# Kernel optimization log

Hardware: AMD Instinct MI355X
Metric: run time of the kernel (lower is better)

## Reference

```python
import jax, jax.numpy as jnp
import numpy as np

KU, H, B, T = 512, 90, 32, 64
ALPHA = 0.5


def setup_inputs() -> dict:
    key = jax.random.key(0)
    ks = jax.random.split(key, 20)
    s = 0.1  # init scale ~ 1/sqrt(H)
    n = lambda k, shape: jax.random.normal(k, shape, jnp.float32) * s
    return {
        "questions": jax.random.randint(ks[0], (B, T), 0, KU),
        "answers": jax.random.randint(ks[1], (B, T), 0, 2 * KU),
        "response_emb": n(ks[2], (2 * KU, H)),
        "concept_emb": n(ks[3], (KU, H)),
        "nb_adj": (jax.random.uniform(ks[4], (KU, KU)) < 0.02).astype(jnp.float32),
        "succ_adj": (jax.random.uniform(ks[5], (KU, KU)) < 0.02).astype(jnp.float32),
        "Wi_self": n(ks[6], (H, 3 * H)), "Wh_self": n(ks[7], (H, 3 * H)),
        "bi_self": jnp.zeros((3 * H,), jnp.float32), "bh_self": jnp.zeros((3 * H,), jnp.float32),
        "Wi_rnn": n(ks[8], (H, 3 * H)), "Wh_rnn": n(ks[9], (H, 3 * H)),
        "bi_rnn": jnp.zeros((3 * H,), jnp.float32), "bh_rnn": jnp.zeros((3 * H,), jnp.float32),
        "W_sync": n(ks[10], (3 * H, H)), "b_sync": jnp.zeros((H,), jnp.float32),
        "W_prop": n(ks[11], (2 * H, H)), "b_prop": jnp.zeros((H,), jnp.float32),
        "W_agg": n(ks[12], (H, H)), "b_agg": jnp.zeros((H,), jnp.float32),
        "W_out": n(ks[13], (H, 1)), "b_out": jnp.zeros((1,), jnp.float32),
    }


def _gru(x, h, Wi, Wh, bi, bh):
    # standard GRU cell; works on [..., H]
    gi = x @ Wi + bi
    gh = h @ Wh + bh
    ir, iz, ig = jnp.split(gi, 3, axis=-1)
    hr, hz, hg = jnp.split(gh, 3, axis=-1)
    r = jax.nn.sigmoid(ir + hr)
    z = jax.nn.sigmoid(iz + hz)
    g = jnp.tanh(ig + r * hg)
    return (1.0 - z) * g + z * h


def reference(questions, answers, response_emb, concept_emb, nb_adj, succ_adj,
              Wi_self, Wh_self, bi_self, bh_self, Wi_rnn, Wh_rnn, bi_rnn, bh_rnn,
              W_sync, b_sync, W_prop, b_prop, W_agg, b_agg, W_out, b_out):
    batch = questions.shape[0]
    ku, hid = concept_emb.shape
    states0 = jnp.zeros((batch, ku, hid), jnp.float32)
    ce = jnp.broadcast_to(concept_emb[None], (batch, ku, hid))  # [B,K,H]
    bidx = jnp.arange(batch)

    def step(states, qa):
        q, a = qa  # [B], [B]
        self_state = states[bidx, q]                               # [B,H] gather
        next_self = _gru(response_emb[a], self_state, Wi_self, Wh_self, bi_self, bh_self)
        self_mask = jax.nn.one_hot(q, ku, dtype=states.dtype)[..., None]   # [B,K,1]
        nb_mask = nb_adj[q][..., None]                                      # [B,K,1]
        # sync: concat(states, broadcast next_self, concept embeds) -> MLP -> neighbor mask
        sync_diff = jnp.concatenate(
            [states, jnp.broadcast_to(next_self[:, None], (batch, ku, hid)), ce], axis=-1)
        sync_inf = nb_mask * jax.nn.relu(sync_diff @ W_sync + b_sync)       # [B,K,H]
        reflec = jnp.sum(sync_inf, axis=1, keepdims=True)                   # [B,1,H]
        sync_inf = sync_inf + self_mask * reflec
        # prop: (delta self state, concept emb of q) -> MLP -> successor mask
        prop_diff = jnp.concatenate([next_self - self_state, concept_emb[q]], axis=-1)  # [B,2H]
        prop_inf = jax.nn.relu(prop_diff @ W_prop + b_prop)                 # [B,H]
        prop_inf = succ_adj[q][..., None] * prop_inf[:, None]               # [B,K,H]
        inf = jax.nn.relu((ALPHA * sync_inf + (1.0 - ALPHA) * prop_inf) @ W_agg + b_agg)
        new_states = _gru(inf, states, Wi_rnn, Wh_rnn, bi_rnn, bh_rnn)      # [B,K,H]
        out = jax.nn.sigmoid(jnp.squeeze(new_states @ W_out + b_out, -1))   # [B,K]
        return new_states, out

    states, outputs = jax.lax.scan(step, states0, (questions.T, answers.T))
    return outputs, states  # outputs: [T,B,K], states: [B,K,H]
```

## Files before the change

kernel.cpp:

```cpp
#include <hip/hip_runtime.h>

#define KU 512
#define NB 32
#define NT 64
#define TIL 64
#define SLOTS 16
#define NBMAX 40

#define N_PONG   (KU * NB * 90)
#define OFF_CEB  (N_PONG)
#define OFF_GI0  (OFF_CEB + KU * 90)
#define OFF_WHTF (OFF_GI0 + 288)
#define OFF_SYF  (OFF_WHTF + 13824)
#define OFF_AGF  (OFF_SYF + 4608)
#define OFF_WIF  (OFF_AGF + 4608)

typedef short bf16x8 __attribute__((ext_vector_type(8)));
typedef float f32x4 __attribute__((ext_vector_type(4)));

__device__ __forceinline__ float sigf(float x) { return 1.0f / (1.0f + __expf(-x)); }
__device__ __forceinline__ float tanhf_(float x) {
    float e = __expf(2.0f * x);
    return 1.0f - 2.0f / (e + 1.0f);
}
__device__ __forceinline__ unsigned short f2bf(float f) {
    union { float f; unsigned u; } v; v.f = f;
    unsigned r = v.u + 0x7FFFu + ((v.u >> 16) & 1u);
    return (unsigned short)(r >> 16);
}
__device__ __forceinline__ bf16x8 cvt8(const float* p) {
    const float4 a0 = *(const float4*)p;
    const float4 a1 = *(const float4*)(p + 4);
    union { bf16x8 v; unsigned short u[8]; } fr;
    fr.u[0] = f2bf(a0.x); fr.u[1] = f2bf(a0.y); fr.u[2] = f2bf(a0.z); fr.u[3] = f2bf(a0.w);
    fr.u[4] = f2bf(a1.x); fr.u[5] = f2bf(a1.y); fr.u[6] = f2bf(a1.z); fr.u[7] = f2bf(a1.w);
    return fr.v;
}

__global__ void skt_prep(const float* __restrict__ concept_emb, const float* __restrict__ W_sync,
                         const float* __restrict__ b_sync, const float* __restrict__ Wi_rnn,
                         const float* __restrict__ Wh_rnn, const float* __restrict__ bi_rnn,
                         const float* __restrict__ b_agg, const float* __restrict__ W_agg,
                         float* __restrict__ ws) {
    const int blk = blockIdx.x, tid = threadIdx.x;
    if (blk < 128) {
        for (int rr = 0; rr < 4; ++rr) {
            const int k = blk * 4 + rr;
            if (tid < 90) {
                float acc = b_sync[tid];
                for (int kk = 0; kk < 90; ++kk)
                    acc += concept_emb[k * 90 + kk] * W_sync[(180 + kk) * 90 + tid];
                ws[OFF_CEB + k * 90 + tid] = acc;
            }
        }
    } else if (blk < 131) {
        const int g = blk - 128;
        unsigned short* p = (unsigned short*)(ws + OFF_WHTF);
        for (int idx = tid; idx < 6 * 3 * 64 * 8; idx += 256) {
            const int i = idx & 7, lane = (idx >> 3) & 63;
            const int rest = idx >> 9;
            const int kk = rest % 3, nb = rest / 3;
            const int n = nb * 16 + (lane & 15);
            const int k = kk * 32 + ((lane >> 4) << 3) + i;
            const float v = (n < 90 && k < 90) ? Wh_rnn[k * 270 + g * 90 + n] : 0.f;
            p[(size_t)g * 9216 + idx] = f2bf(v);
        }
    } else if (blk == 131) {
        for (int c = tid; c < 272; c += 256) {
            float acc = 0.f;
            if (c < 270) {
                acc = bi_rnn[c];
                for (int kk = 0; kk < 90; ++kk)
                    acc += fmaxf(b_agg[kk], 0.f) * Wi_rnn[kk * 270 + c];
            }
            ws[OFF_GI0 + c] = acc;
        }
    } else if (blk == 132) {
        unsigned short* p = (unsigned short*)(ws + OFF_SYF);
        for (int idx = tid; idx < 9216; idx += 256) {
            const int i = idx & 7, lane = (idx >> 3) & 63;
            const int rest = idx >> 9;
            const int kk = rest % 3, nt = rest / 3;
            const int n = nt * 16 + (lane & 15);
            const int k = kk * 32 + ((lane >> 4) << 3) + i;
            p[idx] = f2bf((n < 90 && k < 90) ? W_sync[k * 90 + n] : 0.f);
        }
    } else if (blk == 133) {
        unsigned short* p = (unsigned short*)(ws + OFF_AGF);
        for (int idx = tid; idx < 9216; idx += 256) {
            const int i = idx & 7, lane = (idx >> 3) & 63;
            const int rest = idx >> 9;
            const int kk = rest % 3, nt = rest / 3;
            const int n = nt * 16 + (lane & 15);
            const int k = kk * 32 + ((lane >> 4) << 3) + i;
            p[idx] = f2bf((n < 90 && k < 90) ? W_agg[k * 90 + n] : 0.f);
        }
    } else {
        unsigned short* p = (unsigned short*)(ws + OFF_WIF);
        const int i0 = (blk - 134) * 13824;
        const int i1 = (blk == 134) ? 13824 : 26112;
        for (int idx = i0 + tid; idx < i1; idx += 256) {
            const int i = idx & 7, lane = (idx >> 3) & 63;
            const int rest = idx >> 9;
            const int kk = rest % 3, nt = rest / 3;
            const int n = nt * 16 + (lane & 15);
            const int k = kk * 32 + ((lane >> 4) << 3) + i;
            p[idx] = f2bf((n < 270 && k < 90) ? Wi_rnn[k * 270 + n] : 0.f);
        }
    }
}

__global__ __launch_bounds__(512, 1) void skt_step(
    const int* __restrict__ qs, const int* __restrict__ as_,
    const float* __restrict__ response_emb, const float* __restrict__ concept_emb,
    const float* __restrict__ nb_adj, const float* __restrict__ succ_adj,
    const float* __restrict__ Wi_self, const float* __restrict__ Wh_self,
    const float* __restrict__ bi_self, const float* __restrict__ bh_self,
    const float* __restrict__ bi_rnn, const float* __restrict__ bh_rnn,
    const float* __restrict__ b_agg, const float* __restrict__ W_sync,
    const float* __restrict__ W_prop, const float* __restrict__ b_prop,
    const float* __restrict__ W_out, const float* __restrict__ b_out,
    float* __restrict__ ws, const float* __restrict__ stIn, float* __restrict__ stOut,
    float* __restrict__ out, int t) {
    __shared__ alignas(16) float hR[TIL * 100];
    __shared__ alignas(16) float hnb[NBMAX * 96];
    __shared__ alignas(16) float rfd[NBMAX * 92];
    __shared__ alignas(16) float giL[SLOTS * 273];
    __shared__ alignas(16) float actb[SLOTS * 96], infb[SLOTS * 96];
    __shared__ alignas(16) float giA[272], ghA[272];
    __shared__ alignas(16) float gi0L[273], biL[273], bhL[272];
    __shared__ alignas(16) float re[92], ssv[92], ceq[92], nsv[92], xprop[184];
    __shared__ alignas(16) float nsyL[92], pvL[92], baggL[92], woutL[92];
    __shared__ float nbw[NBMAX];
    __shared__ int nblist[NBMAX];
    __shared__ float nbvL[TIL], svL[TIL];
    __shared__ int rowslotS[TIL], listS[TIL];
    __shared__ int nactS, nnbS;

    const int tid = threadIdx.x;
    const int bb = blockIdx.x >> 3;
    const int k0 = (blockIdx.x & 7) * TIL;
    const int q = qs[bb * NT + t];
    const int a = as_[bb * NT + t];
    const bool owner = (q >= k0 && q < k0 + TIL);

    const int w8 = tid >> 6, lane = tid & 63;
    const int lr = lane & 15, lh = lane >> 4;
    const int rt = w8 & 3, cg = w8 >> 2;

    const unsigned short* whtF = (const unsigned short*)(ws + OFF_WHTF);
    const unsigned short* syF = (const unsigned short*)(ws + OFF_SYF);
    const unsigned short* agF = (const unsigned short*)(ws + OFF_AGF);
    const unsigned short* wiF = (const unsigned short*)(ws + OFF_WIF);

    if (tid < 384) {
        for (int idx = tid; idx < TIL * 50; idx += 384) {
            const int row = idx / 50, c2 = idx - row * 50;
            float2 v = make_float2(0.f, 0.f);
            if (c2 < 45)
                v = ((const float2*)(stIn + ((size_t)(bb * KU + k0 + row)) * 90))[c2];
            *(float2*)&hR[row * 100 + 2 * c2] = v;
        }
    } else if (tid < 448) {
        const int l = tid - 384;
        const int kg = k0 + l;
        const float nv = nb_adj[(size_t)q * KU + kg];
        const float sv = succ_adj[(size_t)q * KU + kg];
        nbvL[l] = nv; svL[l] = sv;
        const bool act = (nv != 0.f) || (sv != 0.f) || (kg == q);
        const unsigned long long mb = __ballot(act);
        const int rank = (int)__popcll(mb & ((1ull << l) - 1ull));
        rowslotS[l] = act ? rank : -1;
        if (act) listS[rank] = l;
        if (l == 0) nactS = (int)__popcll(mb);
    } else {
        const int l = tid - 448;
        int base = 0;
        for (int ch = 0; ch < 8; ++ch) {
            const int kp = ch * 64 + l;
            const float nv = nb_adj[(size_t)q * KU + kp];
            const unsigned long long mb = __ballot(nv != 0.f);
            const int idx = base + (int)__popcll(mb & ((1ull << l) - 1ull));
            if (nv != 0.f && idx < NBMAX) { nblist[idx] = kp; nbw[idx] = nv; }
            base += (int)__popcll(mb);
        }
        if (l == 0) nnbS = (base < NBMAX) ? base : NBMAX;
    }
    for (int j = tid; j < 270; j += 512) {
        if (j < 90) re[j] = response_emb[(size_t)a * 90 + j];
        else if (j < 180) ssv[j - 90] = stIn[((size_t)(bb * KU + q)) * 90 + (j - 90)];
        else ceq[j - 180] = concept_emb[(size_t)q * 90 + (j - 180)];
    }
    for (int c = tid; c < 273; c += 512) {
        gi0L[c] = (c < 272) ? ws[OFF_GI0 + c] : 0.f;
        biL[c] = (c < 270) ? bi_rnn[c] : 0.f;
        if (c < 272) bhL[c] = (c < 270) ? bh_rnn[c] : 0.f;
    }
    for (int m = tid; m < 92; m += 512) {
        baggL[m] = (m < 90) ? b_agg[m] : 0.f;
        woutL[m] = (m < 90) ? W_out[m] : 0.f;
    }
    for (int i = tid; i < SLOTS * 12; i += 512) {
        const int half = i >= SLOTS * 6;
        const int j = half ? i - SLOTS * 6 : i;
        const int slot = j / 6, c = 90 + (j - (j / 6) * 6);
        (half ? infb : actb)[slot * 96 + c] = 0.f;
    }
    __syncthreads();

    if (tid < 270) {
        const int half = tid / 135;
        const int c2 = tid - half * 135;
        const float* W = half ? Wh_self : Wi_self;
        const float* xv = half ? ssv : re;
        const float* bv = half ? bh_self : bi_self;
        float a0 = bv[2 * c2], a1 = bv[2 * c2 + 1];
#pragma unroll 15
        for (int k = 0; k < 90; ++k) {
            const float2 w = *(const float2*)&W[k * 270 + 2 * c2];
            const float x = xv[k];
            a0 += x * w.x; a1 += x * w.y;
        }
        float* dst = half ? ghA : giA;
        dst[2 * c2] = a0; dst[2 * c2 + 1] = a1;
    } else if (owner) {
        const int nnb = nnbS;
        for (int i = tid - 270; i < nnb * 48; i += 242) {
            const int j = i / 48, c2 = i - j * 48;
            float2 v = make_float2(0.f, 0.f);
            if (c2 < 45)
                v = ((const float2*)(stIn + ((size_t)(bb * KU + nblist[j])) * 90))[c2];
            *(float2*)&hnb[j * 96 + 2 * c2] = v;
        }
    }
    f32x4 acc[3][3];
#pragma unroll
    for (int g = 0; g < 3; ++g)
#pragma unroll
        for (int ct = 0; ct < 3; ++ct) acc[g][ct] = f32x4{0.f, 0.f, 0.f, 0.f};
    {
        bf16x8 afr[3];
        const float* ar = &hR[(rt * 16 + lr) * 100];
#pragma unroll
        for (int kk = 0; kk < 3; ++kk) afr[kk] = cvt8(ar + kk * 32 + lh * 8);
#pragma unroll
        for (int g = 0; g < 3; ++g) {
#pragma unroll
            for (int ct = 0; ct < 3; ++ct) {
                const int nb = cg * 3 + ct;
                const unsigned short* bp = whtF + (size_t)(g * 6 + nb) * 1536 + lane * 8;
                acc[g][ct] = __builtin_amdgcn_mfma_f32_16x16x32_bf16(
                    afr[0], *(const bf16x8*)(bp), acc[g][ct], 0, 0, 0);
                acc[g][ct] = __builtin_amdgcn_mfma_f32_16x16x32_bf16(
                    afr[1], *(const bf16x8*)(bp + 512), acc[g][ct], 0, 0, 0);
                acc[g][ct] = __builtin_amdgcn_mfma_f32_16x16x32_bf16(
                    afr[2], *(const bf16x8*)(bp + 1024), acc[g][ct], 0, 0, 0);
            }
        }
    }
    __syncthreads();

    if (tid < 90) {
        const float r = sigf(giA[tid] + ghA[tid]);
        const float z = sigf(giA[90 + tid] + ghA[90 + tid]);
        const float g = tanhf_(giA[180 + tid] + r * ghA[180 + tid]);
        const float ns = (1.f - z) * g + z * ssv[tid];
        nsv[tid] = ns;
        xprop[tid] = ns - ssv[tid];
        xprop[90 + tid] = ceq[tid];
    }
    if (owner) {
        const int nnb = nnbS;
        const int mtc = (nnb + 15) >> 4;
        const int pairs = mtc * 6;
        for (int p = w8; p < pairs; p += 8) {
            const int mt = p / 6, nt = p - mt * 6;
            bf16x8 af[3];
            const int jrow = mt * 16 + lr;
            if (jrow < nnb) {
                const float* rp = &hnb[jrow * 96];
#pragma unroll
                for (int kk = 0; kk < 3; ++kk) af[kk] = cvt8(rp + kk * 32 + lh * 8);
            } else {
                const bf16x8 z = {0, 0, 0, 0, 0, 0, 0, 0};
                af[0] = z; af[1] = z; af[2] = z;
            }
            f32x4 d = f32x4{0.f, 0.f, 0.f, 0.f};
            const unsigned short* bp = syF + (size_t)nt * 1536 + lane * 8;
            d = __builtin_amdgcn_mfma_f32_16x16x32_bf16(af[0], *(const bf16x8*)(bp), d, 0, 0, 0);
            d = __builtin_amdgcn_mfma_f32_16x16x32_bf16(af[1], *(const bf16x8*)(bp + 512), d, 0, 0, 0);
            d = __builtin_amdgcn_mfma_f32_16x16x32_bf16(af[2], *(const bf16x8*)(bp + 1024), d, 0, 0, 0);
#pragma unroll
            for (int r4 = 0; r4 < 4; ++r4) {
                const int j = mt * 16 + lh * 4 + r4;
                const int m = nt * 16 + lr;
                if (j < nnb && m < 90)
                    rfd[j * 92 + m] = d[r4] + ws[OFF_CEB + (size_t)nblist[j] * 90 + m];
            }
        }
    }
    __syncthreads();

    if (tid < 90) {
        float d = 0.f;
#pragma unroll 15
        for (int k = 0; k < 90; ++k) d += nsv[k] * W_sync[(90 + k) * 90 + tid];
        nsyL[tid] = d;
    } else if (tid < 180) {
        const int m = tid - 90;
        float d = b_prop[m];
#pragma unroll 20
        for (int k = 0; k < 180; ++k) d += xprop[k] * W_prop[k * 90 + m];
        pvL[m] = fmaxf(d, 0.f);
    }
    __syncthreads();

    const int nact = nactS;
    const int npass0 = (nact + SLOTS - 1) / SLOTS;
    const int npass = (npass0 > 0) ? npass0 : 1;
    for (int pass = 0; pass < npass; ++pass) {
        const int e0p = pass * SLOTS;
        int e1p = e0p + SLOTS; if (e1p > nact) e1p = nact;
        const int na = e1p - e0p;

        if (w8 < 6 && na > 0) {
            const int nt = w8;
            bf16x8 af[3];
            if (lr < na) {
                const float* rp = &hR[listS[e0p + lr] * 100];
#pragma unroll
                for (int kk = 0; kk < 3; ++kk) af[kk] = cvt8(rp + kk * 32 + lh * 8);
            } else {
                const bf16x8 z = {0, 0, 0, 0, 0, 0, 0, 0};
                af[0] = z; af[1] = z; af[2] = z;
            }
            f32x4 d = f32x4{0.f, 0.f, 0.f, 0.f};
            const unsigned short* bp = syF + (size_t)nt * 1536 + lane * 8;
            d = __builtin_amdgcn_mfma_f32_16x16x32_bf16(af[0], *(const bf16x8*)(bp), d, 0, 0, 0);
            d = __builtin_amdgcn_mfma_f32_16x16x32_bf16(af[1], *(const bf16x8*)(bp + 512), d, 0, 0, 0);
            d = __builtin_amdgcn_mfma_f32_16x16x32_bf16(af[2], *(const bf16x8*)(bp + 1024), d, 0, 0, 0);
            const int m = nt * 16 + lr;
            if (m < 90) {
#pragma unroll
                for (int r4 = 0; r4 < 4; ++r4) {
                    const int slot = lh * 4 + r4;
                    if (slot >= na) continue;
                    const int r = listS[e0p + slot];
                    const float nv = nbvL[r], sv = svL[r];
                    float s = 0.f;
                    if (nv != 0.f)
                        s = nv * fmaxf(nsyL[m] + ws[OFF_CEB + (size_t)(k0 + r) * 90 + m] + d[r4], 0.f);
                    if (k0 + r == q) {
                        const int nnb = nnbS;
                        const float nsym = nsyL[m];
                        for (int j = 0; j < nnb; ++j)
                            s += nbw[j] * fmaxf(nsym + rfd[j * 92 + m], 0.f);
                    }
                    actb[slot * 96 + m] = 0.5f * s + 0.5f * sv * pvL[m];
                }
            }
        }
        __syncthreads();

        if (w8 < 6 && na > 0) {
            const int nt = w8;
            bf16x8 af[3];
            if (lr < na) {
                const float* rp = &actb[lr * 96];
#pragma unroll
                for (int kk = 0; kk < 3; ++kk) af[kk] = cvt8(rp + kk * 32 + lh * 8);
            } else {
                const bf16x8 z = {0, 0, 0, 0, 0, 0, 0, 0};
                af[0] = z; af[1] = z; af[2] = z;
            }
            f32x4 d = f32x4{0.f, 0.f, 0.f, 0.f};
            const unsigned short* bp = agF + (size_t)nt * 1536 + lane * 8;
            d = __builtin_amdgcn_mfma_f32_16x16x32_bf16(af[0], *(const bf16x8*)(bp), d, 0, 0, 0);
            d = __builtin_amdgcn_mfma_f32_16x16x32_bf16(af[1], *(const bf16x8*)(bp + 512), d, 0, 0, 0);
            d = __builtin_amdgcn_mfma_f32_16x16x32_bf16(af[2], *(const bf16x8*)(bp + 1024), d, 0, 0, 0);
            const int m = nt * 16 + lr;
            if (m < 90) {
#pragma unroll
                for (int r4 = 0; r4 < 4; ++r4) {
                    const int slot = lh * 4 + r4;
                    if (slot < na) infb[slot * 96 + m] = fmaxf(baggL[m] + d[r4], 0.f);
                }
            }
        }
        __syncthreads();

        if (na > 0) {
            bf16x8 af[3];
            if (lr < na) {
                const float* rp = &infb[lr * 96];
#pragma unroll
                for (int kk = 0; kk < 3; ++kk) af[kk] = cvt8(rp + kk * 32 + lh * 8);
            } else {
                const bf16x8 z = {0, 0, 0, 0, 0, 0, 0, 0};
                af[0] = z; af[1] = z; af[2] = z;
            }
            for (int nt = w8; nt < 17; nt += 8) {
                f32x4 d = f32x4{0.f, 0.f, 0.f, 0.f};
                const unsigned short* bp = wiF + (size_t)nt * 1536 + lane * 8;
                d = __builtin_amdgcn_mfma_f32_16x16x32_bf16(af[0], *(const bf16x8*)(bp), d, 0, 0, 0);
                d = __builtin_amdgcn_mfma_f32_16x16x32_bf16(af[1], *(const bf16x8*)(bp + 512), d, 0, 0, 0);
                d = __builtin_amdgcn_mfma_f32_16x16x32_bf16(af[2], *(const bf16x8*)(bp + 1024), d, 0, 0, 0);
                const int c = nt * 16 + lr;
                if (c < 270) {
#pragma unroll
                    for (int r4 = 0; r4 < 4; ++r4) {
                        const int slot = lh * 4 + r4;
                        if (slot < na) giL[slot * 273 + c] = biL[c] + d[r4];
                    }
                }
            }
        }
        __syncthreads();

#pragma unroll
        for (int ct = 0; ct < 3; ++ct) {
            const int m = cg * 48 + ct * 16 + lr;
            if (m < 90) {
                const float bhr = bhL[m], bhz = bhL[90 + m], bhg = bhL[180 + m];
#pragma unroll
                for (int r4 = 0; r4 < 4; ++r4) {
                    const int row = rt * 16 + 4 * lh + r4;
                    const int sraw = rowslotS[row];
                    const bool mine = (sraw < 0) ? (pass == 0) : (sraw >= e0p && sraw < e1p);
                    if (!mine) continue;
                    const float* gs = (sraw < 0) ? gi0L : &giL[(sraw - e0p) * 273];
                    const float rg = sigf(gs[m] + acc[0][ct][r4] + bhr);
                    const float zg = sigf(gs[90 + m] + acc[1][ct][r4] + bhz);
                    const float gg = tanhf_(gs[180 + m] + rg * (acc[2][ct][r4] + bhg));
                    const float hold = hR[row * 100 + m];
                    const float hn = (1.f - zg) * gg + zg * hold;
                    hR[row * 100 + m] = hn;
                    stOut[((size_t)(bb * KU + k0 + row)) * 90 + m] = hn;
                }
            }
        }
        __syncthreads();
    }

    {
        const int row = tid >> 3, j = tid & 7;
        const int m0 = j * 12;
        float p = 0.f;
#pragma unroll
        for (int mm = 0; mm < 12; ++mm) {
            const int m = m0 + mm;
            if (m < 90) p += hR[row * 100 + m] * woutL[m];
        }
#pragma unroll
        for (int o = 1; o < 8; o <<= 1) p += __shfl_xor(p, o);
        if (j == 0)
            out[(size_t)t * NB * KU + (size_t)bb * KU + k0 + row] = sigf(p + b_out[0]);
    }
}

extern "C" void kernel_launch(void* const* d_in, const int* in_sizes, int n_in,
                              void* d_out, int out_size, void* d_ws, size_t ws_size,
                              hipStream_t stream) {
    const int* questions = (const int*)d_in[0];
    const int* answers = (const int*)d_in[1];
    const float* response_emb = (const float*)d_in[2];
    const float* concept_emb = (const float*)d_in[3];
    const float* nb_adj = (const float*)d_in[4];
    const float* succ_adj = (const float*)d_in[5];
    const float* Wi_self = (const float*)d_in[6];
    const float* Wh_self = (const float*)d_in[7];
    const float* bi_self = (const float*)d_in[8];
    const float* bh_self = (const float*)d_in[9];
    const float* Wi_rnn = (const float*)d_in[10];
    const float* Wh_rnn = (const float*)d_in[11];
    const float* bi_rnn = (const float*)d_in[12];
    const float* bh_rnn = (const float*)d_in[13];
    const float* W_sync = (const float*)d_in[14];
    const float* b_sync = (const float*)d_in[15];
    const float* W_prop = (const float*)d_in[16];
    const float* b_prop = (const float*)d_in[17];
    const float* W_agg = (const float*)d_in[18];
    const float* b_agg = (const float*)d_in[19];
    const float* W_out = (const float*)d_in[20];
    const float* b_out = (const float*)d_in[21];

    float* out = (float*)d_out;
    float* stFinal = out + (size_t)NT * NB * KU;
    float* ws = (float*)d_ws;

    hipMemsetAsync(stFinal, 0, (size_t)NB * KU * 90 * sizeof(float), stream);
    skt_prep<<<136, 256, 0, stream>>>(concept_emb, W_sync, b_sync, Wi_rnn, Wh_rnn,
                                      bi_rnn, b_agg, W_agg, ws);
    for (int t = 0; t < NT; ++t) {
        const float* sin = (t & 1) ? ws : stFinal;
        float* sout = (t & 1) ? stFinal : ws;
        skt_step<<<NB * 8, 512, 0, stream>>>(
            questions, answers, response_emb, concept_emb, nb_adj, succ_adj,
            Wi_self, Wh_self, bi_self, bh_self, bi_rnn, bh_rnn, b_agg,
            W_sync, W_prop, b_prop, W_out, b_out,
            ws, sin, sout, out, t);
    }
}
```

Baseline: 1.590 ms.

## Halve tile size, double blocks, and move self-GRU and small matvecs to MFMA

```diff
diff --git a/kernel.cpp b/kernel.cpp
--- a/kernel.cpp
+++ b/kernel.cpp
@@ -3,8 +3,8 @@
 #define KU 512
 #define NB 32
 #define NT 64
-#define TIL 64
-#define SLOTS 16
+#define TIL 32
+#define SLOTS 8
 #define NBMAX 40
 
 #define N_PONG   (KU * NB * 90)
@@ -14,6 +14,10 @@
 #define OFF_SYF  (OFF_WHTF + 13824)
 #define OFF_AGF  (OFF_SYF + 4608)
 #define OFF_WIF  (OFF_AGF + 4608)
+#define OFF_WISF (OFF_WIF + 13056)
+#define OFF_WHSF (OFF_WISF + 13056)
+#define OFF_SYMF (OFF_WHSF + 13056)
+#define OFF_WPRF (OFF_SYMF + 4608)
 
 typedef short bf16x8 __attribute__((ext_vector_type(8)));
 typedef float f32x4 __attribute__((ext_vector_type(4)));
@@ -39,9 +43,10 @@
 
 __global__ void skt_prep(const float* __restrict__ concept_emb, const float* __restrict__ W_sync,
                          const float* __restrict__ b_sync, const float* __restrict__ Wi_rnn,
-                         const float* __restrict__ Wh_rnn, const float* __restrict__ bi_rnn,
-                         const float* __restrict__ b_agg, const float* __restrict__ W_agg,
-                         float* __restrict__ ws) {
+                         const float* __restrict__ Wh_rnn, const float* __restrict__ Wi_self,
+                         const float* __restrict__ Wh_self, const float* __restrict__ W_prop,
+                         const float* __restrict__ bi_rnn, const float* __restrict__ b_agg,
+                         const float* __restrict__ W_agg, float* __restrict__ ws) {
     const int blk = blockIdx.x, tid = threadIdx.x;
     if (blk < 128) {
         for (int rr = 0; rr < 4; ++rr) {
@@ -56,14 +61,12 @@
     } else if (blk < 131) {
         const int g = blk - 128;
         unsigned short* p = (unsigned short*)(ws + OFF_WHTF);
-        for (int idx = tid; idx < 6 * 3 * 64 * 8; idx += 256) {
-            const int i = idx & 7, lane = (idx >> 3) & 63;
-            const int rest = idx >> 9;
-            const int kk = rest % 3, nb = rest / 3;
+        for (int idx = tid; idx < 9216; idx += 256) {
+            const int i = idx & 7, lane = (idx >> 3) & 63;
+            const int rest = idx >> 9, kk = rest % 3, nb = rest / 3;
             const int n = nb * 16 + (lane & 15);
             const int k = kk * 32 + ((lane >> 4) << 3) + i;
-            const float v = (n < 90 && k < 90) ? Wh_rnn[k * 270 + g * 90 + n] : 0.f;
-            p[(size_t)g * 9216 + idx] = f2bf(v);
+            p[(size_t)g * 9216 + idx] = f2bf((n < 90 && k < 90) ? Wh_rnn[k * 270 + g * 90 + n] : 0.f);
         }
     } else if (blk == 131) {
         for (int c = tid; c < 272; c += 256) {
@@ -79,8 +82,7 @@
         unsigned short* p = (unsigned short*)(ws + OFF_SYF);
         for (int idx = tid; idx < 9216; idx += 256) {
             const int i = idx & 7, lane = (idx >> 3) & 63;
-            const int rest = idx >> 9;
-            const int kk = rest % 3, nt = rest / 3;
+            const int rest = idx >> 9, kk = rest % 3, nt = rest / 3;
             const int n = nt * 16 + (lane & 15);
             const int k = kk * 32 + ((lane >> 4) << 3) + i;
             p[idx] = f2bf((n < 90 && k < 90) ? W_sync[k * 90 + n] : 0.f);
@@ -89,36 +91,69 @@
         unsigned short* p = (unsigned short*)(ws + OFF_AGF);
         for (int idx = tid; idx < 9216; idx += 256) {
             const int i = idx & 7, lane = (idx >> 3) & 63;
-            const int rest = idx >> 9;
-            const int kk = rest % 3, nt = rest / 3;
+            const int rest = idx >> 9, kk = rest % 3, nt = rest / 3;
             const int n = nt * 16 + (lane & 15);
             const int k = kk * 32 + ((lane >> 4) << 3) + i;
             p[idx] = f2bf((n < 90 && k < 90) ? W_agg[k * 90 + n] : 0.f);
         }
+    } else if (blk < 136) {
+        unsigned short* p = (unsigned short*)(ws + OFF_WIF);
+        const int i0 = (blk - 134) * 13056, i1 = i0 + 13056;
+        for (int idx = i0 + tid; idx < i1; idx += 256) {
+            const int i = idx & 7, lane = (idx >> 3) & 63;
+            const int rest = idx >> 9, kk = rest % 3, nt = rest / 3;
+            const int n = nt * 16 + (lane & 15);
+            const int k = kk * 32 + ((lane >> 4) << 3) + i;
+            p[idx] = f2bf((n < 270 && k < 90) ? Wi_rnn[k * 270 + n] : 0.f);
+        }
+    } else if (blk < 138) {
+        unsigned short* p = (unsigned short*)(ws + OFF_WISF);
+        const int i0 = (blk - 136) * 13056, i1 = i0 + 13056;
+        for (int idx = i0 + tid; idx < i1; idx += 256) {
+            const int i = idx & 7, lane = (idx >> 3) & 63;
+            const int rest = idx >> 9, kk = rest % 3, nt = rest / 3;
+            const int n = nt * 16 + (lane & 15);
+            const int k = kk * 32 + ((lane >> 4) << 3) + i;
+            p[idx] = f2bf((n < 270 && k < 90) ? Wi_self[k * 270 + n] : 0.f);
+        }
+    } else if (blk < 140) {
+        unsigned short* p = (unsigned short*)(ws + OFF_WHSF);
+        const int i0 = (blk - 138) * 13056, i1 = i0 + 13056;
+        for (int idx = i0 + tid; idx < i1; idx += 256) {
+            const int i = idx & 7, lane = (idx >> 3) & 63;
+            const int rest = idx >> 9, kk = rest % 3, nt = rest / 3;
+            const int n = nt * 16 + (lane & 15);
+            const int k = kk * 32 + ((lane >> 4) << 3) + i;
+            p[idx] = f2bf((n < 270 && k < 90) ? Wh_self[k * 270 + n] : 0.f);
+        }
+    } else if (blk == 140) {
+        unsigned short* p = (unsigned short*)(ws + OFF_SYMF);
+        for (int idx = tid; idx < 9216; idx += 256) {
+            const int i = idx & 7, lane = (idx >> 3) & 63;
+            const int rest = idx >> 9, kk = rest % 3, nt = rest / 3;
+            const int n = nt * 16 + (lane & 15);
+            const int k = kk * 32 + ((lane >> 4) << 3) + i;
+            p[idx] = f2bf((n < 90 && k < 90) ? W_sync[(90 + k) * 90 + n] : 0.f);
+        }
     } else {
-        unsigned short* p = (unsigned short*)(ws + OFF_WIF);
-        const int i0 = (blk - 134) * 13824;
-        const int i1 = (blk == 134) ? 13824 : 26112;
-        for (int idx = i0 + tid; idx < i1; idx += 256) {
-            const int i = idx & 7, lane = (idx >> 3) & 63;
-            const int rest = idx >> 9;
-            const int kk = rest % 3, nt = rest / 3;
-            const int n = nt * 16 + (lane & 15);
-            const int k = kk * 32 + ((lane >> 4) << 3) + i;
-            p[idx] = f2bf((n < 270 && k < 90) ? Wi_rnn[k * 270 + n] : 0.f);
+        unsigned short* p = (unsigned short*)(ws + OFF_WPRF);
+        for (int idx = tid; idx < 18432; idx += 256) {
+            const int i = idx & 7, lane = (idx >> 3) & 63;
+            const int rest = idx >> 9, kk = rest % 6, nt = rest / 6;
+            const int n = nt * 16 + (lane & 15);
+            const int k = kk * 32 + ((lane >> 4) << 3) + i;
+            p[idx] = f2bf((n < 90 && k < 180) ? W_prop[k * 90 + n] : 0.f);
         }
     }
 }
 
-__global__ __launch_bounds__(512, 1) void skt_step(
+__global__ __launch_bounds__(256, 2) void skt_step(
     const int* __restrict__ qs, const int* __restrict__ as_,
     const float* __restrict__ response_emb, const float* __restrict__ concept_emb,
     const float* __restrict__ nb_adj, const float* __restrict__ succ_adj,
-    const float* __restrict__ Wi_self, const float* __restrict__ Wh_self,
     const float* __restrict__ bi_self, const float* __restrict__ bh_self,
     const float* __restrict__ bi_rnn, const float* __restrict__ bh_rnn,
-    const float* __restrict__ b_agg, const float* __restrict__ W_sync,
-    const float* __restrict__ W_prop, const float* __restrict__ b_prop,
+    const float* __restrict__ b_agg, const float* __restrict__ b_prop,
     const float* __restrict__ W_out, const float* __restrict__ b_out,
     float* __restrict__ ws, const float* __restrict__ stIn, float* __restrict__ stOut,
     float* __restrict__ out, int t) {
@@ -129,7 +164,7 @@
     __shared__ alignas(16) float actb[SLOTS * 96], infb[SLOTS * 96];
     __shared__ alignas(16) float giA[272], ghA[272];
     __shared__ alignas(16) float gi0L[273], biL[273], bhL[272];
-    __shared__ alignas(16) float re[92], ssv[92], ceq[92], nsv[92], xprop[184];
+    __shared__ alignas(16) float re[96], ssv[96], ceq[92], nsv[96], xprop[192];
     __shared__ alignas(16) float nsyL[92], pvL[92], baggL[92], woutL[92];
     __shared__ float nbw[NBMAX];
     __shared__ int nblist[NBMAX];
@@ -138,43 +173,55 @@
     __shared__ int nactS, nnbS;
 
     const int tid = threadIdx.x;
-    const int bb = blockIdx.x >> 3;
-    const int k0 = (blockIdx.x & 7) * TIL;
+    const int bb = blockIdx.x >> 4;
+    const int k0 = (blockIdx.x & 15) * TIL;
     const int q = qs[bb * NT + t];
     const int a = as_[bb * NT + t];
     const bool owner = (q >= k0 && q < k0 + TIL);
 
-    const int w8 = tid >> 6, lane = tid & 63;
+    const int w4 = tid >> 6, lane = tid & 63;
     const int lr = lane & 15, lh = lane >> 4;
-    const int rt = w8 & 3, cg = w8 >> 2;
+    const int rt = w4 & 1, cg = w4 >> 1;
+    const bf16x8 z8 = {0, 0, 0, 0, 0, 0, 0, 0};
 
     const unsigned short* whtF = (const unsigned short*)(ws + OFF_WHTF);
     const unsigned short* syF = (const unsigned short*)(ws + OFF_SYF);
     const unsigned short* agF = (const unsigned short*)(ws + OFF_AGF);
     const unsigned short* wiF = (const unsigned short*)(ws + OFF_WIF);
-
-    if (tid < 384) {
-        for (int idx = tid; idx < TIL * 50; idx += 384) {
+    const unsigned short* wisF = (const unsigned short*)(ws + OFF_WISF);
+    const unsigned short* whsF = (const unsigned short*)(ws + OFF_WHSF);
+    const unsigned short* symF = (const unsigned short*)(ws + OFF_SYMF);
+    const unsigned short* wprF = (const unsigned short*)(ws + OFF_WPRF);
+
+    if (tid < 128) {
+        for (int idx = tid; idx < TIL * 50; idx += 128) {
             const int row = idx / 50, c2 = idx - row * 50;
             float2 v = make_float2(0.f, 0.f);
             if (c2 < 45)
                 v = ((const float2*)(stIn + ((size_t)(bb * KU + k0 + row)) * 90))[c2];
             *(float2*)&hR[row * 100 + 2 * c2] = v;
         }
-    } else if (tid < 448) {
-        const int l = tid - 384;
-        const int kg = k0 + l;
-        const float nv = nb_adj[(size_t)q * KU + kg];
-        const float sv = succ_adj[(size_t)q * KU + kg];
-        nbvL[l] = nv; svL[l] = sv;
-        const bool act = (nv != 0.f) || (sv != 0.f) || (kg == q);
+    } else if (tid < 192) {
+        const int l = tid - 128;
+        const bool valid = (l < TIL);
+        float nv = 0.f, sv = 0.f;
+        bool act = false;
+        if (valid) {
+            const int kg = k0 + l;
+            nv = nb_adj[(size_t)q * KU + kg];
+            sv = succ_adj[(size_t)q * KU + kg];
+            act = (nv != 0.f) || (sv != 0.f) || (kg == q);
+            nbvL[l] = nv; svL[l] = sv;
+        }
         const unsigned long long mb = __ballot(act);
-        const int rank = (int)__popcll(mb & ((1ull << l) - 1ull));
-        rowslotS[l] = act ? rank : -1;
-        if (act) listS[rank] = l;
-        if (l == 0) nactS = (int)__popcll(mb);
+        if (valid) {
+            const int rank = (int)__popcll(mb & ((1ull << l) - 1ull));
+            rowslotS[l] = act ? rank : -1;
+            if (act) listS[rank] = l;
+            if (l == 0) nactS = (int)__popcll(mb);
+        }
     } else {
-        const int l = tid - 448;
+        const int l = tid - 192;
         int base = 0;
         for (int ch = 0; ch < 8; ++ch) {
             const int kp = ch * 64 + l;
@@ -186,46 +233,33 @@
         }
         if (l == 0) nnbS = (base < NBMAX) ? base : NBMAX;
     }
-    for (int j = tid; j < 270; j += 512) {
+    for (int j = tid; j < 270; j += 256) {
         if (j < 90) re[j] = response_emb[(size_t)a * 90 + j];
         else if (j < 180) ssv[j - 90] = stIn[((size_t)(bb * KU + q)) * 90 + (j - 90)];
         else ceq[j - 180] = concept_emb[(size_t)q * 90 + (j - 180)];
     }
-    for (int c = tid; c < 273; c += 512) {
+    for (int c = tid; c < 273; c += 256) {
         gi0L[c] = (c < 272) ? ws[OFF_GI0 + c] : 0.f;
         biL[c] = (c < 270) ? bi_rnn[c] : 0.f;
         if (c < 272) bhL[c] = (c < 270) ? bh_rnn[c] : 0.f;
     }
-    for (int m = tid; m < 92; m += 512) {
-        baggL[m] = (m < 90) ? b_agg[m] : 0.f;
-        woutL[m] = (m < 90) ? W_out[m] : 0.f;
-    }
-    for (int i = tid; i < SLOTS * 12; i += 512) {
-        const int half = i >= SLOTS * 6;
-        const int j = half ? i - SLOTS * 6 : i;
-        const int slot = j / 6, c = 90 + (j - (j / 6) * 6);
-        (half ? infb : actb)[slot * 96 + c] = 0.f;
+    if (tid < 92) {
+        baggL[tid] = (tid < 90) ? b_agg[tid] : 0.f;
+        woutL[tid] = (tid < 90) ? W_out[tid] : 0.f;
+    } else if (tid < 110) {
+        const int l = tid - 92;
+        if (l < 6) { re[90 + l] = 0.f; ssv[90 + l] = 0.f; nsv[90 + l] = 0.f; }
+        else xprop[180 + (l - 6)] = 0.f;
+    } else if (tid < 206) {
+        const int l = tid - 110;
+        if (l < 48) actb[(l / 6) * 96 + 90 + (l % 6)] = 0.f;
+        else if (l < 96) infb[((l - 48) / 6) * 96 + 90 + ((l - 48) % 6)] = 0.f;
     }
     __syncthreads();
 
-    if (tid < 270) {
-        const int half = tid / 135;
-        const int c2 = tid - half * 135;
-        const float* W = half ? Wh_self : Wi_self;
-        const float* xv = half ? ssv : re;
-        const float* bv = half ? bh_self : bi_self;
-        float a0 = bv[2 * c2], a1 = bv[2 * c2 + 1];
-#pragma unroll 15
-        for (int k = 0; k < 90; ++k) {
-            const float2 w = *(const float2*)&W[k * 270 + 2 * c2];
-            const float x = xv[k];
-            a0 += x * w.x; a1 += x * w.y;
-        }
-        float* dst = half ? ghA : giA;
-        dst[2 * c2] = a0; dst[2 * c2 + 1] = a1;
-    } else if (owner) {
+    if (owner) {
         const int nnb = nnbS;
-        for (int i = tid - 270; i < nnb * 48; i += 242) {
+        for (int i = tid; i < nnb * 48; i += 256) {
             const int j = i / 48, c2 = i - j * 48;
             float2 v = make_float2(0.f, 0.f);
             if (c2 < 45)
@@ -233,6 +267,25 @@
             *(float2*)&hnb[j * 96 + 2 * c2] = v;
         }
     }
+    for (int nt = w4; nt < 17; nt += 4) {
+        bf16x8 af[3];
+#pragma unroll
+        for (int kk = 0; kk < 3; ++kk)
+            af[kk] = (lr == 0) ? cvt8(&re[kk * 32 + lh * 8])
+                   : ((lr == 1) ? cvt8(&ssv[kk * 32 + lh * 8]) : z8);
+        f32x4 dwi = f32x4{0.f, 0.f, 0.f, 0.f}, dwh = f32x4{0.f, 0.f, 0.f, 0.f};
+        const unsigned short* bip = wisF + (size_t)nt * 1536 + lane * 8;
+        const unsigned short* bhp = whsF + (size_t)nt * 1536 + lane * 8;
+#pragma unroll
+        for (int kk = 0; kk < 3; ++kk) {
+            dwi = __builtin_amdgcn_mfma_f32_16x16x32_bf16(af[kk], *(const bf16x8*)(bip + kk * 512), dwi, 0, 0, 0);
+            dwh = __builtin_amdgcn_mfma_f32_16x16x32_bf16(af[kk], *(const bf16x8*)(bhp + kk * 512), dwh, 0, 0, 0);
+        }
+        if (lh == 0) {
+            const int c = nt * 16 + lr;
+            if (c < 270) { giA[c] = bi_self[c] + dwi[0]; ghA[c] = bh_self[c] + dwh[1]; }
+        }
+    }
     f32x4 acc[3][3];
 #pragma unroll
     for (int g = 0; g < 3; ++g)
@@ -249,12 +302,9 @@
             for (int ct = 0; ct < 3; ++ct) {
                 const int nb = cg * 3 + ct;
                 const unsigned short* bp = whtF + (size_t)(g * 6 + nb) * 1536 + lane * 8;
-                acc[g][ct] = __builtin_amdgcn_mfma_f32_16x16x32_bf16(
-                    afr[0], *(const bf16x8*)(bp), acc[g][ct], 0, 0, 0);
-                acc[g][ct] = __builtin_amdgcn_mfma_f32_16x16x32_bf16(
-                    afr[1], *(const bf16x8*)(bp + 512), acc[g][ct], 0, 0, 0);
-                acc[g][ct] = __builtin_amdgcn_mfma_f32_16x16x32_bf16(
-                    afr[2], *(const bf16x8*)(bp + 1024), acc[g][ct], 0, 0, 0);
+                acc[g][ct] = __builtin_amdgcn_mfma_f32_16x16x32_bf16(afr[0], *(const bf16x8*)(bp), acc[g][ct], 0, 0, 0);
+                acc[g][ct] = __builtin_amdgcn_mfma_f32_16x16x32_bf16(afr[1], *(const bf16x8*)(bp + 512), acc[g][ct], 0, 0, 0);
+                acc[g][ct] = __builtin_amdgcn_mfma_f32_16x16x32_bf16(afr[2], *(const bf16x8*)(bp + 1024), acc[g][ct], 0, 0, 0);
             }
         }
     }
@@ -271,9 +321,8 @@
     }
     if (owner) {
         const int nnb = nnbS;
-        const int mtc = (nnb + 15) >> 4;
-        const int pairs = mtc * 6;
-        for (int p = w8; p < pairs; p += 8) {
+        const int pairs = ((nnb + 15) >> 4) * 6;
+        for (int p = w4; p < pairs; p += 4) {
             const int mt = p / 6, nt = p - mt * 6;
             bf16x8 af[3];
             const int jrow = mt * 16 + lr;
@@ -281,10 +330,7 @@
                 const float* rp = &hnb[jrow * 96];
 #pragma unroll
                 for (int kk = 0; kk < 3; ++kk) af[kk] = cvt8(rp + kk * 32 + lh * 8);
-            } else {
-                const bf16x8 z = {0, 0, 0, 0, 0, 0, 0, 0};
-                af[0] = z; af[1] = z; af[2] = z;
-            }
+            } else { af[0] = z8; af[1] = z8; af[2] = z8; }
             f32x4 d = f32x4{0.f, 0.f, 0.f, 0.f};
             const unsigned short* bp = syF + (size_t)nt * 1536 + lane * 8;
             d = __builtin_amdgcn_mfma_f32_16x16x32_bf16(af[0], *(const bf16x8*)(bp), d, 0, 0, 0);
@@ -301,17 +347,24 @@
     }
     __syncthreads();
 
-    if (tid < 90) {
-        float d = 0.f;
-#pragma unroll 15
-        for (int k = 0; k < 90; ++k) d += nsv[k] * W_sync[(90 + k) * 90 + tid];
-        nsyL[tid] = d;
-    } else if (tid < 180) {
-        const int m = tid - 90;
-        float d = b_prop[m];
-#pragma unroll 20
-        for (int k = 0; k < 180; ++k) d += xprop[k] * W_prop[k * 90 + m];
-        pvL[m] = fmaxf(d, 0.f);
+    for (int job = w4; job < 12; job += 4) {
+        const bool isP = job >= 6;
+        const int nt = isP ? job - 6 : job;
+        const float* src = isP ? xprop : nsv;
+        const int nkf = isP ? 6 : 3;
+        const unsigned short* bp = (isP ? wprF + (size_t)nt * 3072 : symF + (size_t)nt * 1536) + lane * 8;
+        f32x4 d = f32x4{0.f, 0.f, 0.f, 0.f};
+        for (int kk = 0; kk < nkf; ++kk) {
+            const bf16x8 av = (lr == 0) ? cvt8(&src[kk * 32 + lh * 8]) : z8;
+            d = __builtin_amdgcn_mfma_f32_16x16x32_bf16(av, *(const bf16x8*)(bp + kk * 512), d, 0, 0, 0);
+        }
+        if (lh == 0) {
+            const int m = nt * 16 + lr;
+            if (m < 90) {
+                if (isP) pvL[m] = fmaxf(b_prop[m] + d[0], 0.f);
+                else nsyL[m] = d[0];
+            }
+        }
     }
     __syncthreads();
 
@@ -323,17 +376,13 @@
         int e1p = e0p + SLOTS; if (e1p > nact) e1p = nact;
         const int na = e1p - e0p;
 
-        if (w8 < 6 && na > 0) {
-            const int nt = w8;
+        if (na > 0) for (int nt = w4; nt < 6; nt += 4) {
             bf16x8 af[3];
             if (lr < na) {
                 const float* rp = &hR[listS[e0p + lr] * 100];
 #pragma unroll
                 for (int kk = 0; kk < 3; ++kk) af[kk] = cvt8(rp + kk * 32 + lh * 8);
-            } else {
-                const bf16x8 z = {0, 0, 0, 0, 0, 0, 0, 0};
-                af[0] = z; af[1] = z; af[2] = z;
-            }
+            } else { af[0] = z8; af[1] = z8; af[2] = z8; }
             f32x4 d = f32x4{0.f, 0.f, 0.f, 0.f};
             const unsigned short* bp = syF + (size_t)nt * 1536 + lane * 8;
             d = __builtin_amdgcn_mfma_f32_16x16x32_bf16(af[0], *(const bf16x8*)(bp), d, 0, 0, 0);
@@ -362,17 +411,13 @@
         }
         __syncthreads();
 
-        if (w8 < 6 && na > 0) {
-            const int nt = w8;
+        if (na > 0) for (int nt = w4; nt < 6; nt += 4) {
             bf16x8 af[3];
             if (lr < na) {
                 const float* rp = &actb[lr * 96];
 #pragma unroll
                 for (int kk = 0; kk < 3; ++kk) af[kk] = cvt8(rp + kk * 32 + lh * 8);
-            } else {
-                const bf16x8 z = {0, 0, 0, 0, 0, 0, 0, 0};
-                af[0] = z; af[1] = z; af[2] = z;
-            }
+            } else { af[0] = z8; af[1] = z8; af[2] = z8; }
             f32x4 d = f32x4{0.f, 0.f, 0.f, 0.f};
             const unsigned short* bp = agF + (size_t)nt * 1536 + lane * 8;
             d = __builtin_amdgcn_mfma_f32_16x16x32_bf16(af[0], *(const bf16x8*)(bp), d, 0, 0, 0);
@@ -395,11 +440,8 @@
                 const float* rp = &infb[lr * 96];
 #pragma unroll
                 for (int kk = 0; kk < 3; ++kk) af[kk] = cvt8(rp + kk * 32 + lh * 8);
-            } else {
-                const bf16x8 z = {0, 0, 0, 0, 0, 0, 0, 0};
-                af[0] = z; af[1] = z; af[2] = z;
-            }
-            for (int nt = w8; nt < 17; nt += 8) {
+            } else { af[0] = z8; af[1] = z8; af[2] = z8; }
+            for (int nt = w4; nt < 17; nt += 4) {
                 f32x4 d = f32x4{0.f, 0.f, 0.f, 0.f};
                 const unsigned short* bp = wiF + (size_t)nt * 1536 + lane * 8;
                 d = __builtin_amdgcn_mfma_f32_16x16x32_bf16(af[0], *(const bf16x8*)(bp), d, 0, 0, 0);
@@ -489,15 +531,14 @@
     float* ws = (float*)d_ws;
 
     hipMemsetAsync(stFinal, 0, (size_t)NB * KU * 90 * sizeof(float), stream);
-    skt_prep<<<136, 256, 0, stream>>>(concept_emb, W_sync, b_sync, Wi_rnn, Wh_rnn,
-                                      bi_rnn, b_agg, W_agg, ws);
+    skt_prep<<<142, 256, 0, stream>>>(concept_emb, W_sync, b_sync, Wi_rnn, Wh_rnn,
+                                      Wi_self, Wh_self, W_prop, bi_rnn, b_agg, W_agg, ws);
     for (int t = 0; t < NT; ++t) {
         const float* sin = (t & 1) ? ws : stFinal;
         float* sout = (t & 1) ? stFinal : ws;
-        skt_step<<<NB * 8, 512, 0, stream>>>(
+        skt_step<<<NB * 16, 256, 0, stream>>>(
             questions, answers, response_emb, concept_emb, nb_adj, succ_adj,
-            Wi_self, Wh_self, bi_self, bh_self, bi_rnn, bh_rnn, b_agg,
-            W_sync, W_prop, b_prop, W_out, b_out,
+            bi_self, bh_self, bi_rnn, bh_rnn, b_agg, b_prop, W_out, b_out,
             ws, sin, sout, out, t);
     }
 }
```

After: 2.064 ms. 29.8% more time.
